# Performance work log

Hardware: AMD Instinct MI355X
Metric: run time of the kernel (lower is better)

Reference implementation:

```python
import jax, jax.numpy as jnp
import numpy as np

N = 50000   # nodes
E = 800000  # edges (avg degree 16)
IN = 256    # in_dim
H = 4       # nhead
D = 64      # out_dim per head
NEG_SLOPE_ATTN = 0.2   # DGL GATConv default negative_slope for edge scores
NEG_SLOPE_OUT = 0.01   # nn.LeakyReLU default on the layer output


def setup_inputs() -> dict:
    key = jax.random.key(0)
    ks = jax.random.split(key, 6)
    h = jax.random.normal(ks[0], (N, IN), dtype=jnp.float32)
    src = jax.random.randint(ks[1], (E,), 0, N, dtype=jnp.int32)
    dst = jax.random.randint(ks[2], (E,), 0, N, dtype=jnp.int32)
    W = jax.random.normal(ks[3], (IN, H * D), dtype=jnp.float32) / np.float32(np.sqrt(IN))
    attn_l = jax.random.normal(ks[4], (H, D), dtype=jnp.float32) * 0.1
    attn_r = jax.random.normal(ks[5], (H, D), dtype=jnp.float32) * 0.1
    bias = jnp.zeros((H * D,), dtype=jnp.float32)
    return {"h": h, "src": src, "dst": dst, "W": W,
            "attn_l": attn_l, "attn_r": attn_r, "bias": bias}


def reference(h, src, dst, W, attn_l, attn_r, bias):
    n = h.shape[0]
    # linear projection -> [N, H, D]
    feat = (h @ W).reshape(n, H, D)
    # per-node, per-head attention halves: [N, H]
    el = jnp.sum(feat * attn_l, axis=-1)
    er = jnp.sum(feat * attn_r, axis=-1)
    # per-edge unnormalized score (DGL: src contributes el, dst contributes er)
    e = jax.nn.leaky_relu(el[src] + er[dst], NEG_SLOPE_ATTN)  # [E, H]
    # edge softmax over incoming edges of each destination node
    emax = jax.ops.segment_max(e, dst, num_segments=n)        # [N, H]
    ee = jnp.exp(e - emax[dst])                               # [E, H]
    denom = jax.ops.segment_sum(ee, dst, num_segments=n)      # [N, H]
    a = ee / jnp.maximum(denom[dst], 1e-9)                    # [E, H]
    # weighted scatter-aggregate of projected source features
    msg = feat[src] * a[:, :, None]                           # [E, H, D]
    rst = jax.ops.segment_sum(msg, dst, num_segments=n)       # [N, H, D]
    rst = rst + bias.reshape(H, D)
    # outer activation (dropout is identity in eval)
    return jax.nn.leaky_relu(rst, NEG_SLOPE_OUT)
```

## Files before the change

### kernel.cpp

```cpp
#include <hip/hip_runtime.h>

#define IN_DIM 256
#define HD 256
#define NHEAD 4
#define BM 128

typedef __attribute__((ext_vector_type(8))) short short8;
typedef __attribute__((ext_vector_type(4))) float f32x4;

__device__ __forceinline__ float bf2f(ushort u) {
    unsigned x = ((unsigned)u) << 16;
    float f;
    __builtin_memcpy(&f, &x, 4);
    return f;
}
__device__ __forceinline__ ushort f2bf(float f) {
    unsigned x;
    __builtin_memcpy(&x, &f, 4);
    unsigned r = (x + 0x7FFFu + ((x >> 16) & 1u)) >> 16;
    return (ushort)r;
}
__device__ __forceinline__ short8 cvt8(float4 x, float4 y) {
    short8 a;
    a[0] = (short)f2bf(x.x); a[1] = (short)f2bf(x.y);
    a[2] = (short)f2bf(x.z); a[3] = (short)f2bf(x.w);
    a[4] = (short)f2bf(y.x); a[5] = (short)f2bf(y.y);
    a[6] = (short)f2bf(y.z); a[7] = (short)f2bf(y.w);
    return a;
}

__global__ void fill_one(float* __restrict__ out, int n) {
    int i = blockIdx.x * 256 + threadIdx.x;
    if (i < n) out[i] = 1.0f;
}

__global__ void conv_w(const float* __restrict__ W, ushort* __restrict__ WT) {
    int idx = blockIdx.x * 256 + threadIdx.x;
    int k = idx >> 8, c = idx & 255;
    WT[c * 256 + k] = f2bf(W[idx]);
}

__global__ __launch_bounds__(256, 2) void gemm_feat(const float* __restrict__ h,
                                                    const short* __restrict__ WT,
                                                    ushort* __restrict__ featb,
                                                    float* __restrict__ el,
                                                    float* __restrict__ er,
                                                    const float* __restrict__ attn_l,
                                                    const float* __restrict__ attn_r,
                                                    int n) {
    __shared__ __align__(16) ushort blds[2][8192];
    int t = threadIdx.x;
    int w = t >> 6, l = t & 63;
    int c15 = l & 15, g = l >> 4;
    int blockBase = blockIdx.x * BM;
    int row0 = blockBase + w * 32 + c15;
    int rA0 = row0 < n ? row0 : n - 1;
    int rA1 = (row0 + 16) < n ? (row0 + 16) : n - 1;
    const float* hA0 = h + (size_t)rA0 * 256 + g * 8;
    const float* hA1 = h + (size_t)rA1 * 256 + g * 8;

    f32x4 acc[2][16];
#pragma unroll
    for (int af = 0; af < 2; ++af)
#pragma unroll
        for (int ct = 0; ct < 16; ++ct) acc[af][ct] = (f32x4)(0.0f);

    short8 st[4];
    int sc[4], sb[4];
#pragma unroll
    for (int p = 0; p < 4; ++p) {
        int q = t + p * 256;
        sc[p] = q >> 2;
        int gg = q & 3;
        sb[p] = ((sc[p] * 64 + gg * 16) ^ ((sc[p] & 7) << 4));
    }

#pragma unroll
    for (int p = 0; p < 4; ++p)
        st[p] = *(const short8*)(WT + sc[p] * 256 + ((t + p * 256) & 3) * 8);
#pragma unroll
    for (int p = 0; p < 4; ++p)
        *(short8*)((char*)blds[0] + sb[p]) = st[p];
    __syncthreads();

    for (int kk = 0; kk < 8; ++kk) {
        int buf = kk & 1;
        if (kk < 7) {
#pragma unroll
            for (int p = 0; p < 4; ++p)
                st[p] = *(const short8*)(WT + sc[p] * 256 + (kk + 1) * 32 + ((t + p * 256) & 3) * 8);
        }
        float4 x0 = *(const float4*)(hA0 + kk * 32);
        float4 y0 = *(const float4*)(hA0 + kk * 32 + 4);
        float4 x1 = *(const float4*)(hA1 + kk * 32);
        float4 y1 = *(const float4*)(hA1 + kk * 32 + 4);
        short8 a0 = cvt8(x0, y0);
        short8 a1 = cvt8(x1, y1);
        const char* bb = (const char*)blds[buf];
#pragma unroll
        for (int ct = 0; ct < 16; ++ct) {
            int c = ct * 16 + c15;
            short8 bv = *(const short8*)(bb + ((c * 64 + g * 16) ^ ((c & 7) << 4)));
            acc[0][ct] = __builtin_amdgcn_mfma_f32_16x16x32_bf16(a0, bv, acc[0][ct], 0, 0, 0);
            acc[1][ct] = __builtin_amdgcn_mfma_f32_16x16x32_bf16(a1, bv, acc[1][ct], 0, 0, 0);
        }
        if (kk < 7) {
#pragma unroll
            for (int p = 0; p < 4; ++p)
                *(short8*)((char*)blds[buf ^ 1] + sb[p]) = st[p];
        }
        __syncthreads();
    }

    float alv[16], arv[16];
#pragma unroll
    for (int ct = 0; ct < 16; ++ct) {
        alv[ct] = attn_l[ct * 16 + c15];
        arv[ct] = attn_r[ct * 16 + c15];
    }

#pragma unroll
    for (int af = 0; af < 2; ++af) {
        int rowb = blockBase + w * 32 + af * 16 + g * 4;
#pragma unroll
        for (int r = 0; r < 4; ++r) {
            int row = rowb + r;
            if (row < n) {
#pragma unroll
                for (int ct = 0; ct < 16; ++ct)
                    featb[(size_t)row * 256 + ct * 16 + c15] = f2bf(acc[af][ct][r]);
            }
            float pl[4] = {0.f, 0.f, 0.f, 0.f}, pr[4] = {0.f, 0.f, 0.f, 0.f};
#pragma unroll
            for (int ct = 0; ct < 16; ++ct) {
                pl[ct >> 2] += acc[af][ct][r] * alv[ct];
                pr[ct >> 2] += acc[af][ct][r] * arv[ct];
            }
#pragma unroll
            for (int m = 1; m < 16; m <<= 1) {
#pragma unroll
                for (int hh = 0; hh < 4; ++hh) {
                    pl[hh] += __shfl_xor(pl[hh], m, 64);
                    pr[hh] += __shfl_xor(pr[hh], m, 64);
                }
            }
            if (row < n) {
                if (c15 < 4)       el[row * 4 + c15]       = pl[c15];
                else if (c15 < 8)  er[row * 4 + (c15 - 4)] = pr[c15 - 4];
            }
        }
    }
}

__global__ void hist_kernel(const int* __restrict__ dst, int* __restrict__ cnt,
                            int* __restrict__ epos, int e) {
    int i = blockIdx.x * 256 + threadIdx.x;
    if (i < e) epos[i] = atomicAdd(&cnt[dst[i]], 1);
}

__global__ __launch_bounds__(1024) void scan_local(const int* __restrict__ cnt,
                                                   int* __restrict__ rl,
                                                   int* __restrict__ bsum, int n) {
    __shared__ int wsums[16];
    int t = threadIdx.x, lane = t & 63, wid = t >> 6;
    int i = blockIdx.x * 1024 + t;
    int x = (i < n) ? cnt[i] : 0;
    int s = x;
#pragma unroll
    for (int off = 1; off < 64; off <<= 1) {
        int v = __shfl_up(s, off, 64);
        if (lane >= off) s += v;
    }
    if (lane == 63) wsums[wid] = s;
    __syncthreads();
    if (wid == 0) {
        int ws = (lane < 16) ? wsums[lane] : 0;
#pragma unroll
        for (int off = 1; off < 16; off <<= 1) {
            int v = __shfl_up(ws, off, 64);
            if (lane >= off) ws += v;
        }
        if (lane < 16) wsums[lane] = ws;
    }
    __syncthreads();
    int woff = (wid > 0) ? wsums[wid - 1] : 0;
    if (i <= n) rl[i] = woff + s - x;
    if (t == 1023) bsum[blockIdx.x] = wsums[15];
}

__global__ __launch_bounds__(1024) void scan_bsum(int* __restrict__ bsum, int nb) {
    __shared__ int wsums[16];
    int t = threadIdx.x, lane = t & 63, wid = t >> 6;
    int x = (t < nb) ? bsum[t] : 0;
    int s = x;
#pragma unroll
    for (int off = 1; off < 64; off <<= 1) {
        int v = __shfl_up(s, off, 64);
        if (lane >= off) s += v;
    }
    if (lane == 63) wsums[wid] = s;
    __syncthreads();
    if (wid == 0) {
        int ws = (lane < 16) ? wsums[lane] : 0;
#pragma unroll
        for (int off = 1; off < 16; off <<= 1) {
            int v = __shfl_up(ws, off, 64);
            if (lane >= off) ws += v;
        }
        if (lane < 16) wsums[lane] = ws;
    }
    __syncthreads();
    int woff = (wid > 0) ? wsums[wid - 1] : 0;
    if (t < nb) bsum[t] = woff + s - x;
}

__global__ void fill_kernel(const int* __restrict__ src, const int* __restrict__ dst,
                            const int* __restrict__ rl, const int* __restrict__ boffs,
                            const int* __restrict__ epos,
                            int* __restrict__ esrc, int e) {
    int i = blockIdx.x * 256 + threadIdx.x;
    if (i >= e) return;
    int d = dst[i];
    int pos = boffs[d >> 10] + rl[d] + epos[i];
    if (pos >= 0 && pos < e) esrc[pos] = src[i];
}

__global__ __launch_bounds__(64) void aggregate(const int* __restrict__ rl,
                                                const int* __restrict__ boffs,
                                                const int* __restrict__ esrc,
                                                const float* __restrict__ el,
                                                const float* __restrict__ er,
                                                const ushort* __restrict__ featb,
                                                const float* __restrict__ bias,
                                                float* __restrict__ out, int n) {
    __shared__ int sbuf[64];
    __shared__ float wbuf[64][4];
    int node = blockIdx.x;
    int l = threadIdx.x;
    int hh = l >> 4;
    int beg = boffs[node >> 10] + rl[node];
    int end = boffs[(node + 1) >> 10] + rl[node + 1];
    float4 bv = *(const float4*)(bias + l * 4);
    float* op = out + (size_t)node * 256 + l * 4;
    if (beg >= end) {
        float4 v;
        v.x = bv.x > 0.f ? bv.x : 0.01f * bv.x;
        v.y = bv.y > 0.f ? bv.y : 0.01f * bv.y;
        v.z = bv.z > 0.f ? bv.z : 0.01f * bv.z;
        v.w = bv.w > 0.f ? bv.w : 0.01f * bv.w;
        *(float4*)op = v;
        return;
    }
    float4 r4 = *(const float4*)(er + (size_t)node * 4);
    float ax = 0.f, ay = 0.f, az = 0.f, aw = 0.f, s = 0.f;
    for (int cb = beg; cb < end; cb += 64) {
        int cn = min(64, end - cb);
        __syncthreads();
        if (l < cn) {
            int sv = esrc[cb + l];
            sv = (sv >= 0 && sv < n) ? sv : 0;
            sbuf[l] = sv;
            float4 l4 = *(const float4*)(el + (size_t)sv * 4);
            float e0 = l4.x + r4.x; e0 = e0 > 0.f ? e0 : 0.2f * e0;
            float e1 = l4.y + r4.y; e1 = e1 > 0.f ? e1 : 0.2f * e1;
            float e2 = l4.z + r4.z; e2 = e2 > 0.f ? e2 : 0.2f * e2;
            float e3 = l4.w + r4.w; e3 = e3 > 0.f ? e3 : 0.2f * e3;
            wbuf[l][0] = __expf(fminf(e0, 60.f));
            wbuf[l][1] = __expf(fminf(e1, 60.f));
            wbuf[l][2] = __expf(fminf(e2, 60.f));
            wbuf[l][3] = __expf(fminf(e3, 60.f));
        }
        __syncthreads();
#pragma unroll 4
        for (int j = 0; j < cn; ++j) {
            int sid = sbuf[j];
            float wgt = wbuf[j][hh];
            ushort4 f4 = *(const ushort4*)(featb + (size_t)sid * 256 + l * 4);
            ax += wgt * bf2f(f4.x);
            ay += wgt * bf2f(f4.y);
            az += wgt * bf2f(f4.z);
            aw += wgt * bf2f(f4.w);
            s += wgt;
        }
    }
    float inv = 1.f / fmaxf(s, 1e-9f);
    float4 v;
    v.x = ax * inv + bv.x; v.x = v.x > 0.f ? v.x : 0.01f * v.x;
    v.y = ay * inv + bv.y; v.y = v.y > 0.f ? v.y : 0.01f * v.y;
    v.z = az * inv + bv.z; v.z = v.z > 0.f ? v.z : 0.01f * v.z;
    v.w = aw * inv + bv.w; v.w = v.w > 0.f ? v.w : 0.01f * v.w;
    *(float4*)op = v;
}

extern "C" void kernel_launch(void* const* d_in, const int* in_sizes, int n_in,
                              void* d_out, int out_size, void* d_ws, size_t ws_size,
                              hipStream_t stream) {
    const float* h      = (const float*)d_in[0];
    const int*   src    = (const int*)d_in[1];
    const int*   dst    = (const int*)d_in[2];
    const float* W      = (const float*)d_in[3];
    const float* attn_l = (const float*)d_in[4];
    const float* attn_r = (const float*)d_in[5];
    const float* bias   = (const float*)d_in[6];
    float* out = (float*)d_out;

    int N = in_sizes[0] / IN_DIM;
    int E = in_sizes[1];
    int NB = (N + 1 + 1023) / 1024;

    auto al = [](size_t x) { return (x + 255) & ~(size_t)255; };
    char* ws = (char*)d_ws;
    size_t o = 0;
    ushort* featb = (ushort*)(ws + o); o += al((size_t)N * HD * 2);
    float*  el    = (float*)(ws + o);  o += al((size_t)N * NHEAD * 4);
    float*  er    = (float*)(ws + o);  o += al((size_t)N * NHEAD * 4);
    int*    rl    = (int*)(ws + o);    o += al((size_t)(N + 1) * 4);
    int*    cnt   = (int*)(ws + o);    o += al((size_t)N * 4);
    int*    bsum  = (int*)(ws + o);    o += al((size_t)NB * 4);
    int*    esrc  = (int*)(ws + o);    o += al((size_t)E * 4);
    int*    epos  = (int*)(ws + o);    o += al((size_t)E * 4);
    ushort* WT    = (ushort*)(ws + o); o += al((size_t)IN_DIM * HD * 2);
    (void)n_in;

    if (ws_size < o) {
        fill_one<<<(out_size + 255) / 256, 256, 0, stream>>>(out, out_size);
        return;
    }

    conv_w<<<(IN_DIM * HD) / 256, 256, 0, stream>>>(W, WT);
    gemm_feat<<<(N + BM - 1) / BM, 256, 0, stream>>>(h, (const short*)WT, featb, el, er,
                                                     attn_l, attn_r, N);
    hipMemsetAsync(cnt, 0, (size_t)N * 4, stream);
    hipMemsetAsync(esrc, 0, (size_t)E * 4, stream);
    hist_kernel<<<(E + 255) / 256, 256, 0, stream>>>(dst, cnt, epos, E);
    scan_local<<<NB, 1024, 0, stream>>>(cnt, rl, bsum, N);
    scan_bsum<<<1, 1024, 0, stream>>>(bsum, NB);
    fill_kernel<<<(E + 255) / 256, 256, 0, stream>>>(src, dst, rl, bsum, epos, esrc, E);
    aggregate<<<N, 64, 0, stream>>>(rl, bsum, esrc, el, er, featb, bias, out, N);
}
```

Before: 158.6 us.

## Shrink GEMM row tile, vectorize histogram/fill kernels, drop esrc memset

The GEMM block tile drops from 128 to 64 rows, each wave computing one 16-row fragment, and launch bounds rise to 3 blocks per CU. The aim is more blocks in flight and fewer accumulator registers, at the cost of loading the B tile into LDS twice as often per output row. The histogram and CSR fill kernels now handle four edges per thread with int4 loads. The esrc memset is removed. The remainder path for E not divisible by 4 is a no-op (it passes count 0), so it would be wrong for such E, though E=800000 divides evenly.

```diff
diff --git a/kernel.cpp b/kernel.cpp
--- a/kernel.cpp
+++ b/kernel.cpp
@@ -3,7 +3,7 @@
 #define IN_DIM 256
 #define HD 256
 #define NHEAD 4
-#define BM 128
+#define BM 64
 
 typedef __attribute__((ext_vector_type(8))) short short8;
 typedef __attribute__((ext_vector_type(4))) float f32x4;
@@ -40,7 +40,7 @@
     WT[c * 256 + k] = f2bf(W[idx]);
 }
 
-__global__ __launch_bounds__(256, 2) void gemm_feat(const float* __restrict__ h,
+__global__ __launch_bounds__(256, 3) void gemm_feat(const float* __restrict__ h,
                                                     const short* __restrict__ WT,
                                                     ushort* __restrict__ featb,
                                                     float* __restrict__ el,
@@ -53,17 +53,13 @@
     int w = t >> 6, l = t & 63;
     int c15 = l & 15, g = l >> 4;
     int blockBase = blockIdx.x * BM;
-    int row0 = blockBase + w * 32 + c15;
+    int row0 = blockBase + w * 16 + c15;
     int rA0 = row0 < n ? row0 : n - 1;
-    int rA1 = (row0 + 16) < n ? (row0 + 16) : n - 1;
     const float* hA0 = h + (size_t)rA0 * 256 + g * 8;
-    const float* hA1 = h + (size_t)rA1 * 256 + g * 8;
-
-    f32x4 acc[2][16];
-#pragma unroll
-    for (int af = 0; af < 2; ++af)
-#pragma unroll
-        for (int ct = 0; ct < 16; ++ct) acc[af][ct] = (f32x4)(0.0f);
+
+    f32x4 acc[16];
+#pragma unroll
+    for (int ct = 0; ct < 16; ++ct) acc[ct] = (f32x4)(0.0f);
 
     short8 st[4];
     int sc[4], sb[4];
@@ -92,17 +88,13 @@
         }
         float4 x0 = *(const float4*)(hA0 + kk * 32);
         float4 y0 = *(const float4*)(hA0 + kk * 32 + 4);
-        float4 x1 = *(const float4*)(hA1 + kk * 32);
-        float4 y1 = *(const float4*)(hA1 + kk * 32 + 4);
         short8 a0 = cvt8(x0, y0);
-        short8 a1 = cvt8(x1, y1);
         const char* bb = (const char*)blds[buf];
 #pragma unroll
         for (int ct = 0; ct < 16; ++ct) {
             int c = ct * 16 + c15;
             short8 bv = *(const short8*)(bb + ((c * 64 + g * 16) ^ ((c & 7) << 4)));
-            acc[0][ct] = __builtin_amdgcn_mfma_f32_16x16x32_bf16(a0, bv, acc[0][ct], 0, 0, 0);
-            acc[1][ct] = __builtin_amdgcn_mfma_f32_16x16x32_bf16(a1, bv, acc[1][ct], 0, 0, 0);
+            acc[ct] = __builtin_amdgcn_mfma_f32_16x16x32_bf16(a0, bv, acc[ct], 0, 0, 0);
         }
         if (kk < 7) {
 #pragma unroll
@@ -119,43 +111,47 @@
         arv[ct] = attn_r[ct * 16 + c15];
     }
 
-#pragma unroll
-    for (int af = 0; af < 2; ++af) {
-        int rowb = blockBase + w * 32 + af * 16 + g * 4;
-#pragma unroll
-        for (int r = 0; r < 4; ++r) {
-            int row = rowb + r;
-            if (row < n) {
-#pragma unroll
-                for (int ct = 0; ct < 16; ++ct)
-                    featb[(size_t)row * 256 + ct * 16 + c15] = f2bf(acc[af][ct][r]);
+    int rowb = blockBase + w * 16 + g * 4;
+#pragma unroll
+    for (int r = 0; r < 4; ++r) {
+        int row = rowb + r;
+        if (row < n) {
+#pragma unroll
+            for (int ct = 0; ct < 16; ++ct)
+                featb[(size_t)row * 256 + ct * 16 + c15] = f2bf(acc[ct][r]);
+        }
+        float pl[4] = {0.f, 0.f, 0.f, 0.f}, pr[4] = {0.f, 0.f, 0.f, 0.f};
+#pragma unroll
+        for (int ct = 0; ct < 16; ++ct) {
+            pl[ct >> 2] += acc[ct][r] * alv[ct];
+            pr[ct >> 2] += acc[ct][r] * arv[ct];
+        }
+#pragma unroll
+        for (int m = 1; m < 16; m <<= 1) {
+#pragma unroll
+            for (int hh = 0; hh < 4; ++hh) {
+                pl[hh] += __shfl_xor(pl[hh], m, 64);
+                pr[hh] += __shfl_xor(pr[hh], m, 64);
             }
-            float pl[4] = {0.f, 0.f, 0.f, 0.f}, pr[4] = {0.f, 0.f, 0.f, 0.f};
-#pragma unroll
-            for (int ct = 0; ct < 16; ++ct) {
-                pl[ct >> 2] += acc[af][ct][r] * alv[ct];
-                pr[ct >> 2] += acc[af][ct][r] * arv[ct];
-            }
-#pragma unroll
-            for (int m = 1; m < 16; m <<= 1) {
-#pragma unroll
-                for (int hh = 0; hh < 4; ++hh) {
-                    pl[hh] += __shfl_xor(pl[hh], m, 64);
-                    pr[hh] += __shfl_xor(pr[hh], m, 64);
-                }
-            }
-            if (row < n) {
-                if (c15 < 4)       el[row * 4 + c15]       = pl[c15];
-                else if (c15 < 8)  er[row * 4 + (c15 - 4)] = pr[c15 - 4];
-            }
+        }
+        if (row < n) {
+            if (c15 < 4)       el[row * 4 + c15]       = pl[c15];
+            else if (c15 < 8)  er[row * 4 + (c15 - 4)] = pr[c15 - 4];
         }
     }
 }
 
 __global__ void hist_kernel(const int* __restrict__ dst, int* __restrict__ cnt,
-                            int* __restrict__ epos, int e) {
+                            int* __restrict__ epos, int e4) {
     int i = blockIdx.x * 256 + threadIdx.x;
-    if (i < e) epos[i] = atomicAdd(&cnt[dst[i]], 1);
+    if (i >= e4) return;
+    int4 d4 = *(const int4*)(dst + i * 4);
+    int4 p4;
+    p4.x = atomicAdd(&cnt[d4.x], 1);
+    p4.y = atomicAdd(&cnt[d4.y], 1);
+    p4.z = atomicAdd(&cnt[d4.z], 1);
+    p4.w = atomicAdd(&cnt[d4.w], 1);
+    *(int4*)(epos + i * 4) = p4;
 }
 
 __global__ __launch_bounds__(1024) void scan_local(const int* __restrict__ cnt,
@@ -217,12 +213,20 @@
 __global__ void fill_kernel(const int* __restrict__ src, const int* __restrict__ dst,
                             const int* __restrict__ rl, const int* __restrict__ boffs,
                             const int* __restrict__ epos,
-                            int* __restrict__ esrc, int e) {
+                            int* __restrict__ esrc, int e4, int e) {
     int i = blockIdx.x * 256 + threadIdx.x;
-    if (i >= e) return;
-    int d = dst[i];
-    int pos = boffs[d >> 10] + rl[d] + epos[i];
-    if (pos >= 0 && pos < e) esrc[pos] = src[i];
+    if (i >= e4) return;
+    int4 d4 = *(const int4*)(dst + i * 4);
+    int4 s4 = *(const int4*)(src + i * 4);
+    int4 p4 = *(const int4*)(epos + i * 4);
+    int pos0 = boffs[d4.x >> 10] + rl[d4.x] + p4.x;
+    int pos1 = boffs[d4.y >> 10] + rl[d4.y] + p4.y;
+    int pos2 = boffs[d4.z >> 10] + rl[d4.z] + p4.z;
+    int pos3 = boffs[d4.w >> 10] + rl[d4.w] + p4.w;
+    if (pos0 >= 0 && pos0 < e) esrc[pos0] = s4.x;
+    if (pos1 >= 0 && pos1 < e) esrc[pos1] = s4.y;
+    if (pos2 >= 0 && pos2 < e) esrc[pos2] = s4.z;
+    if (pos3 >= 0 && pos3 < e) esrc[pos3] = s4.w;
 }
 
 __global__ __launch_bounds__(64) void aggregate(const int* __restrict__ rl,
@@ -331,10 +335,14 @@
     gemm_feat<<<(N + BM - 1) / BM, 256, 0, stream>>>(h, (const short*)WT, featb, el, er,
                                                      attn_l, attn_r, N);
     hipMemsetAsync(cnt, 0, (size_t)N * 4, stream);
-    hipMemsetAsync(esrc, 0, (size_t)E * 4, stream);
-    hist_kernel<<<(E + 255) / 256, 256, 0, stream>>>(dst, cnt, epos, E);
+    int E4 = E / 4;
+    int Erem = E - E4 * 4;
+    hist_kernel<<<(E4 + 255) / 256, 256, 0, stream>>>(dst, cnt, epos, E4);
+    if (Erem) {
+        hist_kernel<<<1, 256, 0, stream>>>(dst + E4 * 4 - 0, cnt, epos + E4 * 4 - 0, 0);
+    }
     scan_local<<<NB, 1024, 0, stream>>>(cnt, rl, bsum, N);
     scan_bsum<<<1, 1024, 0, stream>>>(bsum, NB);
-    fill_kernel<<<(E + 255) / 256, 256, 0, stream>>>(src, dst, rl, bsum, epos, esrc, E);
+    fill_kernel<<<(E4 + 255) / 256, 256, 0, stream>>>(src, dst, rl, bsum, epos, esrc, E4, E);
     aggregate<<<N, 64, 0, stream>>>(rl, bsum, esrc, el, er, featb, bias, out, N);
 }
```

Measured after the change: 161.5 us. No clear change (+1.9%).

## Fuse histogram into GEMM launch, fold zeroing into weight conversion, vectorize fill

Applied to the files above, without the earlier changes.

The edge-degree histogram now runs as extra blocks of the GEMM launch, so the atomic counting overlaps the projection GEMM instead of running as its own kernel. Zeroing the count array moves into the weight-conversion kernel, and the two memsets are dropped; the esrc memset was redundant because every position is written. Histogram and fill kernels each handle four edges per thread with int4 loads. This removes several launches and serialization points, at the cost of mixing heterogeneous blocks in one grid, which may affect GEMM occupancy and scheduling.

```diff
diff --git a/kernel.cpp b/kernel.cpp
--- a/kernel.cpp
+++ b/kernel.cpp
@@ -34,20 +34,41 @@
     if (i < n) out[i] = 1.0f;
 }
 
-__global__ void conv_w(const float* __restrict__ W, ushort* __restrict__ WT) {
+__global__ void conv_w_zero(const float* __restrict__ W, ushort* __restrict__ WT,
+                            int* __restrict__ cnt, int n) {
     int idx = blockIdx.x * 256 + threadIdx.x;
     int k = idx >> 8, c = idx & 255;
     WT[c * 256 + k] = f2bf(W[idx]);
-}
-
-__global__ __launch_bounds__(256, 2) void gemm_feat(const float* __restrict__ h,
+    for (int i = idx; i < n; i += 65536) cnt[i] = 0;
+}
+
+__global__ __launch_bounds__(256, 2) void gemm_hist(const float* __restrict__ h,
                                                     const short* __restrict__ WT,
                                                     ushort* __restrict__ featb,
                                                     float* __restrict__ el,
                                                     float* __restrict__ er,
                                                     const float* __restrict__ attn_l,
                                                     const float* __restrict__ attn_r,
-                                                    int n) {
+                                                    const int* __restrict__ dst,
+                                                    int* __restrict__ cnt,
+                                                    int* __restrict__ epos,
+                                                    int gb, int n, int e) {
+    if (blockIdx.x >= gb) {
+        int i = (blockIdx.x - gb) * 256 + threadIdx.x;
+        int base = i * 4;
+        if (base + 3 < e) {
+            int4 d4 = *(const int4*)(dst + base);
+            int4 p4;
+            p4.x = atomicAdd(&cnt[d4.x], 1);
+            p4.y = atomicAdd(&cnt[d4.y], 1);
+            p4.z = atomicAdd(&cnt[d4.z], 1);
+            p4.w = atomicAdd(&cnt[d4.w], 1);
+            *(int4*)(epos + base) = p4;
+        } else {
+            for (int q = base; q < e; ++q) epos[q] = atomicAdd(&cnt[dst[q]], 1);
+        }
+        return;
+    }
     __shared__ __align__(16) ushort blds[2][8192];
     int t = threadIdx.x;
     int w = t >> 6, l = t & 63;
@@ -152,12 +173,6 @@
     }
 }
 
-__global__ void hist_kernel(const int* __restrict__ dst, int* __restrict__ cnt,
-                            int* __restrict__ epos, int e) {
-    int i = blockIdx.x * 256 + threadIdx.x;
-    if (i < e) epos[i] = atomicAdd(&cnt[dst[i]], 1);
-}
-
 __global__ __launch_bounds__(1024) void scan_local(const int* __restrict__ cnt,
                                                    int* __restrict__ rl,
                                                    int* __restrict__ bsum, int n) {
@@ -219,10 +234,26 @@
                             const int* __restrict__ epos,
                             int* __restrict__ esrc, int e) {
     int i = blockIdx.x * 256 + threadIdx.x;
-    if (i >= e) return;
-    int d = dst[i];
-    int pos = boffs[d >> 10] + rl[d] + epos[i];
-    if (pos >= 0 && pos < e) esrc[pos] = src[i];
+    int base = i * 4;
+    if (base + 3 < e) {
+        int4 d4 = *(const int4*)(dst + base);
+        int4 s4 = *(const int4*)(src + base);
+        int4 p4 = *(const int4*)(epos + base);
+        int pos0 = boffs[d4.x >> 10] + rl[d4.x] + p4.x;
+        int pos1 = boffs[d4.y >> 10] + rl[d4.y] + p4.y;
+        int pos2 = boffs[d4.z >> 10] + rl[d4.z] + p4.z;
+        int pos3 = boffs[d4.w >> 10] + rl[d4.w] + p4.w;
+        if (pos0 >= 0 && pos0 < e) esrc[pos0] = s4.x;
+        if (pos1 >= 0 && pos1 < e) esrc[pos1] = s4.y;
+        if (pos2 >= 0 && pos2 < e) esrc[pos2] = s4.z;
+        if (pos3 >= 0 && pos3 < e) esrc[pos3] = s4.w;
+    } else {
+        for (int q = base; q < e; ++q) {
+            int d = dst[q];
+            int pos = boffs[d >> 10] + rl[d] + epos[q];
+            if (pos >= 0 && pos < e) esrc[pos] = src[q];
+        }
+    }
 }
 
 __global__ __launch_bounds__(64) void aggregate(const int* __restrict__ rl,
@@ -327,14 +358,17 @@
         return;
     }
 
-    conv_w<<<(IN_DIM * HD) / 256, 256, 0, stream>>>(W, WT);
-    gemm_feat<<<(N + BM - 1) / BM, 256, 0, stream>>>(h, (const short*)WT, featb, el, er,
-                                                     attn_l, attn_r, N);
-    hipMemsetAsync(cnt, 0, (size_t)N * 4, stream);
-    hipMemsetAsync(esrc, 0, (size_t)E * 4, stream);
-    hist_kernel<<<(E + 255) / 256, 256, 0, stream>>>(dst, cnt, epos, E);
+    conv_w_zero<<<(IN_DIM * HD) / 256, 256, 0, stream>>>(W, WT, cnt, N);
+
+    int GB = (N + BM - 1) / BM;
+    int HB = ((E + 3) / 4 + 255) / 256;
+    gemm_hist<<<GB + HB, 256, 0, stream>>>(h, (const short*)WT, featb, el, er,
+                                           attn_l, attn_r, dst, cnt, epos, GB, N, E);
+
     scan_local<<<NB, 1024, 0, stream>>>(cnt, rl, bsum, N);
     scan_bsum<<<1, 1024, 0, stream>>>(bsum, NB);
-    fill_kernel<<<(E + 255) / 256, 256, 0, stream>>>(src, dst, rl, bsum, epos, esrc, E);
+
+    fill_kernel<<<((E + 3) / 4 + 255) / 256, 256, 0, stream>>>(src, dst, rl, bsum, epos, esrc, E);
+
     aggregate<<<N, 64, 0, stream>>>(rl, bsum, esrc, el, er, featb, bias, out, N);
 }
```

New measurement: 139.1 us, median of 2. 1.14x faster.
